# Optimization experiments

Measured on AMD Instinct MI355X. Metric: run time of the kernel, lower is better.

## Reference

```python
import math
import jax, jax.numpy as jnp
import numpy as np

B, H, SQ, SKV, DM = 4, 16, 1024, 1024, 1024
K = 17  # k+1 relative slots
DK = DM // H


def setup_inputs() -> dict:
    key = jax.random.key(0)
    ks = jax.random.split(key, 14)
    n = jax.random.normal
    w_scale = 1.0 / math.sqrt(DM)
    return {
        "query": n(ks[0], (B, SQ, DM), jnp.float32),
        "key": n(ks[1], (B, SKV, DM), jnp.float32),
        "value": n(ks[2], (B, SKV, DM), jnp.float32),
        "pos_enc": n(ks[3], (B, H, K, SKV), jnp.float32),
        "pos_pad": n(ks[4], (B, H, K, SKV), jnp.float32),
        "cross_pos_enc": n(ks[5], (B, H, K, SQ), jnp.float32),
        "cross_pos_pad": n(ks[6], (B, H, K, SQ), jnp.float32),
        "rel_q": n(ks[7], (1, H, 2 * K, DK), jnp.float32) * 0.02,
        "rel_k": n(ks[8], (1, H, 2 * K, DK), jnp.float32) * 0.02,
        "rel_v": n(ks[9], (1, H, 2 * K, DK), jnp.float32) * 0.02,
        "Wq": n(ks[10], (DM, DM), jnp.float32) * w_scale,
        "Wk": n(ks[11], (DM, DM), jnp.float32) * w_scale,
        "Wv": n(ks[12], (DM, DM), jnp.float32) * w_scale,
        "Wo": n(ks[13], (DM, DM), jnp.float32) * w_scale,
    }


def _heads(x, W):
    # nn.Linear(bias=False): y = x @ W.T, then transpose_for_scores -> [B,H,S,DK]
    y = x @ W.T
    b, s, _ = y.shape
    return y.reshape(b, s, H, DK).transpose(0, 2, 1, 3)


def reference(query, key, value, pos_enc, pos_pad, cross_pos_enc, cross_pos_pad,
              rel_q, rel_k, rel_v, Wq, Wk, Wv, Wo):
    q = _heads(query, Wq)   # [B,H,SQ,DK]
    k = _heads(key, Wk)     # [B,H,SKV,DK]
    v = _heads(value, Wv)   # [B,H,SKV,DK]

    # split rel tables: first K rows pair with *_enc, last K rows with *_pad
    rk_e, rk_p = rel_k[0, :, :K], rel_k[0, :, K:]
    rq_e, rq_p = rel_q[0, :, :K], rel_q[0, :, K:]
    rv_e, rv_p = rel_v[0, :, :K], rel_v[0, :, K:]

    # content scores + rel-position bias terms, all [B,H,SQ,SKV]
    scores = jnp.einsum('bhqd,bhsd->bhqs', q, k)
    scores += jnp.einsum('bhqd,hrd,bhrs->bhqs', q, rk_e, pos_enc)
    scores += jnp.einsum('bhqd,hrd,bhrs->bhqs', q, rk_p, pos_pad)
    scores += jnp.einsum('bhsd,hrd,bhrq->bhqs', k, rq_e, cross_pos_enc)
    scores += jnp.einsum('bhsd,hrd,bhrq->bhqs', k, rq_p, cross_pos_pad)

    attn = jax.nn.softmax(scores / math.sqrt(DK), axis=-1)

    out = jnp.einsum('bhqs,bhsd->bhqd', attn, v)
    out += jnp.einsum('bhqs,bhrs,hrd->bhqd', attn, pos_enc, rv_e)
    out += jnp.einsum('bhqs,bhrs,hrd->bhqd', attn, pos_pad, rv_p)

    # finalize_output: merge heads then out_proj
    out = out.transpose(0, 2, 1, 3).reshape(B, SQ, DM)
    return out @ Wo.T
```

## Files before the change

kernel.cpp:

```cpp
#include <hip/hip_runtime.h>
#include <hip/hip_bf16.h>
#include <stdint.h>

typedef float f32x4 __attribute__((ext_vector_type(4)));
typedef __bf16 bf16x8 __attribute__((ext_vector_type(8)));

#define NBH 64
#define SS 1024
#define DAUG 160
#define KAPPA 0.18033688011104293f

static __device__ __forceinline__ unsigned short f2b(float f) {
  union { float f; uint32_t u; } v; v.f = f;
  return (unsigned short)((v.u + 0x7fffu + ((v.u >> 16) & 1u)) >> 16);
}
static __device__ __forceinline__ float b2f(unsigned short s) {
  union { uint32_t u; float f; } v; v.u = ((uint32_t)s) << 16;
  return v.f;
}

static __device__ __forceinline__ void async16(const void* g, void* l) {
  __builtin_amdgcn_global_load_lds(
      (const __attribute__((address_space(1))) uint32_t*)g,
      (__attribute__((address_space(3))) uint32_t*)l, 16, 0, 0);
}

template <int CTRL>
static __device__ __forceinline__ float dppmaxstep(float x) {
  int y = __builtin_amdgcn_update_dpp(__builtin_bit_cast(int, x), __builtin_bit_cast(int, x),
                                      CTRL, 0xF, 0xF, false);
  return fmaxf(x, __builtin_bit_cast(float, y));
}
static __device__ __forceinline__ float rowmax16(float x) {
  x = dppmaxstep<0x128>(x);
  x = dppmaxstep<0x124>(x);
  x = dppmaxstep<0x122>(x);
  x = dppmaxstep<0x121>(x);
  return x;
}

__global__ void convert7(const float* q, const float* k, const float* v,
                         const float* wq, const float* wk, const float* wv, const float* wo,
                         unsigned short* xq, unsigned short* xk, unsigned short* xv,
                         unsigned short* bwq, unsigned short* bwk, unsigned short* bwv,
                         unsigned short* bwo) {
  const float* s; unsigned short* d; int n;
  switch (blockIdx.y) {
    case 0: s = q;  d = xq;  n = 4194304; break;
    case 1: s = k;  d = xk;  n = 4194304; break;
    case 2: s = v;  d = xv;  n = 4194304; break;
    case 3: s = wq; d = bwq; n = 1048576; break;
    case 4: s = wk; d = bwk; n = 1048576; break;
    case 5: s = wv; d = bwv; n = 1048576; break;
    default: s = wo; d = bwo; n = 1048576; break;
  }
  int n4 = n >> 2;
  for (int i = blockIdx.x * blockDim.x + threadIdx.x; i < n4; i += gridDim.x * blockDim.x) {
    float4 f = ((const float4*)s)[i];
    ushort4 o;
    o.x = f2b(f.x); o.y = f2b(f.y); o.z = f2b(f.z); o.w = f2b(f.w);
    ((ushort4*)d)[i] = o;
  }
}

__global__ __launch_bounds__(256) void proj_qkv(
    const unsigned short* __restrict__ Xq, const unsigned short* __restrict__ Xk,
    const unsigned short* __restrict__ Xv, const unsigned short* __restrict__ Wqb,
    const unsigned short* __restrict__ Wkb, const unsigned short* __restrict__ Wvb,
    unsigned short* __restrict__ Qt, unsigned short* __restrict__ Kt,
    unsigned short* __restrict__ Vp) {
  const int z = blockIdx.z;
  const unsigned short* A = (z == 0) ? Xq : (z == 1) ? Xk : Xv;
  const unsigned short* Bw = (z == 0) ? Wqb : (z == 1) ? Wkb : Wvb;
  unsigned short* Dst = (z == 0) ? Qt : (z == 1) ? Kt : Vp;
  const int dstride = (z == 2) ? 64 : DAUG;
  const float sc = (z == 0) ? KAPPA : 1.0f;

  __shared__ unsigned short At[2][128 * 32];
  __shared__ unsigned short Bt[2][128 * 32];

  const int tid = threadIdx.x, wave = tid >> 6, lane = tid & 63;
  const int r15 = lane & 15, g4 = lane >> 4;
  const int i0 = blockIdx.x * 128, j0 = blockIdx.y * 128;
  const int wm = (wave >> 1) * 64, wn = (wave & 1) * 64;

  auto stage = [&](int k0, int buf) {
#pragma unroll
    for (int c = 0; c < 2; ++c) {
      int ch = (wave * 2 + c) * 64 + lane;
      int row = ch >> 2, cg = ch & 3;
      async16(A + (size_t)(i0 + row) * 1024 + k0 + cg * 8, &At[buf][0] + (wave * 2 + c) * 512);
      async16(Bw + (size_t)(j0 + row) * 1024 + k0 + cg * 8, &Bt[buf][0] + (wave * 2 + c) * 512);
    }
  };

  f32x4 acc[4][4];
#pragma unroll
  for (int m = 0; m < 4; ++m)
#pragma unroll
    for (int n = 0; n < 4; ++n) acc[m][n] = (f32x4){0.f, 0.f, 0.f, 0.f};

  stage(0, 0);
  __syncthreads();

  for (int it = 0; it < 32; ++it) {
    const int cur = it & 1, nxt = cur ^ 1;
    if (it < 31) stage((it + 1) * 32, nxt);
    bf16x8 af[4], bf[4];
#pragma unroll
    for (int m = 0; m < 4; ++m)
      af[m] = *(const bf16x8*)(&At[cur][(wm + m * 16 + r15) * 32 + g4 * 8]);
#pragma unroll
    for (int n = 0; n < 4; ++n)
      bf[n] = *(const bf16x8*)(&Bt[cur][(wn + n * 16 + r15) * 32 + g4 * 8]);
    __builtin_amdgcn_s_setprio(1);
#pragma unroll
    for (int m = 0; m < 4; ++m)
#pragma unroll
      for (int n = 0; n < 4; ++n)
        acc[m][n] = __builtin_amdgcn_mfma_f32_16x16x32_bf16(af[m], bf[n], acc[m][n], 0, 0, 0);
    __builtin_amdgcn_s_setprio(0);
    __syncthreads();
  }

#pragma unroll
  for (int m = 0; m < 4; ++m)
#pragma unroll
    for (int n = 0; n < 4; ++n)
#pragma unroll
      for (int r = 0; r < 4; ++r) {
        int i = i0 + wm + m * 16 + g4 * 4 + r;
        int j = j0 + wn + n * 16 + r15;
        int b = i >> 10, s = i & 1023, h = j >> 6, d = j & 63;
        Dst[(((size_t)b * 16 + h) * SS + s) * dstride + d] = f2b(acc[m][n][r] * sc);
      }
}

__global__ __launch_bounds__(256) void gemm_out(const unsigned short* __restrict__ Oh,
                                                const unsigned short* __restrict__ Wob,
                                                float* __restrict__ Out) {
  __shared__ unsigned short At[2][128 * 32];
  __shared__ unsigned short Bt[2][128 * 32];

  const int tid = threadIdx.x, wave = tid >> 6, lane = tid & 63;
  const int r15 = lane & 15, g4 = lane >> 4;
  const int i0 = blockIdx.x * 128, j0 = blockIdx.y * 128;
  const int wm = (wave >> 1) * 64, wn = (wave & 1) * 64;

  auto stage = [&](int k0, int buf) {
#pragma unroll
    for (int c = 0; c < 2; ++c) {
      int ch = (wave * 2 + c) * 64 + lane;
      int row = ch >> 2, cg = ch & 3;
      int i = i0 + row, b = i >> 10, s = i & 1023;
      int kcol = k0 + cg * 8, h = kcol >> 6, dd = kcol & 63;
      async16(Oh + (((size_t)b * 16 + h) * SS + s) * 64 + dd, &At[buf][0] + (wave * 2 + c) * 512);
      async16(Wob + (size_t)(j0 + row) * 1024 + k0 + cg * 8, &Bt[buf][0] + (wave * 2 + c) * 512);
    }
  };

  f32x4 acc[4][4];
#pragma unroll
  for (int m = 0; m < 4; ++m)
#pragma unroll
    for (int n = 0; n < 4; ++n) acc[m][n] = (f32x4){0.f, 0.f, 0.f, 0.f};

  stage(0, 0);
  __syncthreads();

  for (int it = 0; it < 32; ++it) {
    const int cur = it & 1, nxt = cur ^ 1;
    if (it < 31) stage((it + 1) * 32, nxt);
    bf16x8 af[4], bf[4];
#pragma unroll
    for (int m = 0; m < 4; ++m)
      af[m] = *(const bf16x8*)(&At[cur][(wm + m * 16 + r15) * 32 + g4 * 8]);
#pragma unroll
    for (int n = 0; n < 4; ++n)
      bf[n] = *(const bf16x8*)(&Bt[cur][(wn + n * 16 + r15) * 32 + g4 * 8]);
    __builtin_amdgcn_s_setprio(1);
#pragma unroll
    for (int m = 0; m < 4; ++m)
#pragma unroll
      for (int n = 0; n < 4; ++n)
        acc[m][n] = __builtin_amdgcn_mfma_f32_16x16x32_bf16(af[m], bf[n], acc[m][n], 0, 0, 0);
    __builtin_amdgcn_s_setprio(0);
    __syncthreads();
  }

#pragma unroll
  for (int m = 0; m < 4; ++m)
#pragma unroll
    for (int n = 0; n < 4; ++n)
#pragma unroll
      for (int r = 0; r < 4; ++r) {
        int i = i0 + wm + m * 16 + g4 * 4 + r;
        int j = j0 + wn + n * 16 + r15;
        Out[(size_t)i * 1024 + j] = acc[m][n][r];
      }
}

__global__ __launch_bounds__(256) void aug_dots_mfma2(unsigned short* __restrict__ Qt,
                                                      unsigned short* __restrict__ Kt,
                                                      const float* __restrict__ relk,
                                                      const float* __restrict__ relq) {
  const int z = blockIdx.z;
  unsigned short* T = z ? Kt : Qt;
  const float* rel = z ? relq : relk;
  const int cbase = z ? 98 : 64;
  const int bh = blockIdx.y, h = bh & 15, s0 = blockIdx.x * 128;
  const int tid = threadIdx.x, wave = tid >> 6, lane = tid & 63;
  const int r15 = lane & 15, g4 = lane >> 4;

  __shared__ unsigned short RL[48 * 72];
  for (int idx = tid; idx < 48 * 64; idx += 256) {
    int r = idx >> 6, d = idx & 63;
    RL[r * 72 + d] = (r < 34) ? f2b(rel[((size_t)h * 34 + r) * 64 + d]) : (unsigned short)0;
  }
  __syncthreads();

  bf16x8 bfr[3][2];
#pragma unroll
  for (int n = 0; n < 3; ++n)
#pragma unroll
    for (int st = 0; st < 2; ++st)
      bfr[n][st] = *(const bf16x8*)(RL + (n * 16 + r15) * 72 + st * 32 + g4 * 8);

  f32x4 acc[2][3];
#pragma unroll
  for (int m = 0; m < 2; ++m)
#pragma unroll
    for (int n = 0; n < 3; ++n) acc[m][n] = (f32x4){0.f, 0.f, 0.f, 0.f};

#pragma unroll
  for (int m = 0; m < 2; ++m) {
    const unsigned short* Arow = T + ((size_t)bh * SS + s0 + wave * 32 + m * 16 + r15) * DAUG;
    bf16x8 a0 = *(const bf16x8*)(Arow + g4 * 8);
    bf16x8 a1 = *(const bf16x8*)(Arow + 32 + g4 * 8);
#pragma unroll
    for (int n = 0; n < 3; ++n) {
      acc[m][n] = __builtin_amdgcn_mfma_f32_16x16x32_bf16(a0, bfr[n][0], acc[m][n], 0, 0, 0);
      acc[m][n] = __builtin_amdgcn_mfma_f32_16x16x32_bf16(a1, bfr[n][1], acc[m][n], 0, 0, 0);
    }
  }

#pragma unroll
  for (int m = 0; m < 2; ++m)
#pragma unroll
    for (int n = 0; n < 3; ++n) {
      int col = n * 16 + r15;
      if (col < 34) {
#pragma unroll
        for (int r = 0; r < 4; ++r) {
          int row = s0 + wave * 32 + m * 16 + g4 * 4 + r;
          T[((size_t)bh * SS + row) * DAUG + cbase + col] = f2b(acc[m][n][r]);
        }
      }
    }
}

__global__ __launch_bounds__(256) void pos_copy2(unsigned short* __restrict__ Qt,
                                                 unsigned short* __restrict__ Kt,
                                                 const float* __restrict__ cpe,
                                                 const float* __restrict__ cpp,
                                                 const float* __restrict__ pe,
                                                 const float* __restrict__ pp) {
  const int z = blockIdx.z;
  unsigned short* T = z ? Kt : Qt;
  const float* Pe = z ? pe : cpe;
  const float* Pp = z ? pp : cpp;
  const int cbase = z ? 64 : 98;
  const float scale = z ? 1.0f : KAPPA;
  const int bh = blockIdx.y, s0 = blockIdx.x * 64;
  const int tid = threadIdx.x;
  __shared__ float PeL[17][65];
  __shared__ float PpL[17][65];

  for (int idx = tid; idx < 17 * 64; idx += 256) {
    int r = idx >> 6, c = idx & 63;
    PeL[r][c] = Pe[((size_t)bh * 17 + r) * SS + s0 + c];
    PpL[r][c] = Pp[((size_t)bh * 17 + r) * SS + s0 + c];
  }
  __syncthreads();

  for (int idx = tid; idx < 4096; idx += 256) {
    int s = idx >> 6, j = idx & 63;
    if (j < 34) {
      float v = (j < 17) ? PeL[j][s] : PpL[j - 17][s];
      T[((size_t)bh * SS + s0 + s) * DAUG + cbase + j] = f2b(v * scale);
    } else if (j < 62) {
      T[((size_t)bh * SS + s0 + s) * DAUG + 132 + (j - 34)] = 0;
    }
  }
}

__global__ __launch_bounds__(256) void vprime_T(const unsigned short* __restrict__ Vp,
                                                const float* __restrict__ Pe,
                                                const float* __restrict__ Pp,
                                                const float* __restrict__ relv,
                                                unsigned short* __restrict__ VpT) {
  const int bh = blockIdx.y, h = bh & 15, s0 = blockIdx.x * 64;
  const int tid = threadIdx.x;
  __shared__ float PeL[17][65];
  __shared__ float PpL[17][65];
  __shared__ unsigned short VT[64][72];

  for (int idx = tid; idx < 17 * 64; idx += 256) {
    int r = idx >> 6, c = idx & 63;
    PeL[r][c] = Pe[((size_t)bh * 17 + r) * SS + s0 + c];
    PpL[r][c] = Pp[((size_t)bh * 17 + r) * SS + s0 + c];
  }
  __syncthreads();

  const int d = tid & 63, sg = tid >> 6;
  float acc[16];
#pragma unroll
  for (int si = 0; si < 16; ++si) acc[si] = 0.f;
  for (int r = 0; r < 17; ++r) {
    float ve = relv[((size_t)h * 34 + r) * 64 + d];
    float vpv = relv[((size_t)h * 34 + 17 + r) * 64 + d];
#pragma unroll
    for (int si = 0; si < 16; ++si) {
      int s = sg * 16 + si;
      acc[si] += PeL[r][s] * ve + PpL[r][s] * vpv;
    }
  }
#pragma unroll
  for (int si = 0; si < 16; ++si) {
    int s = sg * 16 + si;
    float v = b2f(Vp[((size_t)bh * SS + s0 + s) * 64 + d]) + acc[si];
    VT[d][s] = f2b(v);
  }
  __syncthreads();

  for (int c = tid; c < 512; c += 256) {
    int row = c >> 3, c8 = c & 7;
    uint4 v = *(const uint4*)&VT[row][c8 * 8];
    *(uint4*)(VpT + ((size_t)bh * 80 + row) * 1024 + s0 + c8 * 8) = v;
  }
  if (tid < 128) {
    int row = 64 + (tid >> 3), c8 = tid & 7;
    uint32_t w = (row == 64) ? 0x3F803F80u : 0u;
    uint4 v = {w, w, w, w};
    *(uint4*)(VpT + ((size_t)bh * 80 + row) * 1024 + s0 + c8 * 8) = v;
  }
}

__global__ __launch_bounds__(512, 4) void flash_attn3(
    const unsigned short* __restrict__ Qt, const unsigned short* __restrict__ Kt,
    const unsigned short* __restrict__ VpT, unsigned short* __restrict__ Oh) {
  const int bh = blockIdx.y;
  const int q0 = blockIdx.x * 128;
  const int tid = threadIdx.x, wave = tid >> 6, lane = tid & 63;
  const int r15 = lane & 15, g4 = lane >> 4;

  __shared__ unsigned short Ks[2][64 * 160];
  __shared__ unsigned short Vs[2][80 * 64];
  __shared__ unsigned short Ps[128 * 72];

  const unsigned short* Kbase = Kt + (size_t)bh * SS * DAUG;
  const unsigned short* Vbase = VpT + (size_t)bh * 80 * 1024;

  bf16x8 qf[5];
  {
    const unsigned short* Qg = Qt + ((size_t)bh * SS + q0 + wave * 16 + r15) * DAUG;
#pragma unroll
    for (int kk = 0; kk < 5; ++kk) qf[kk] = *(const bf16x8*)(Qg + kk * 32 + g4 * 8);
  }

  auto stageK = [&](int kv0, int buf) {
    const unsigned short* Kg = Kbase + (size_t)kv0 * DAUG;
#pragma unroll
    for (int j = 0; j < 2; ++j) {
      int ibase = j * 512 + wave * 64;
      int i = ibase + lane;
      int row = i / 20, c = i % 20;
      int cs = (c < 16) ? (c ^ (row & 7)) : (16 + ((c & 3) ^ (row & 3)));
      async16(Kg + (size_t)row * DAUG + cs * 8, &Ks[buf][0] + (size_t)ibase * 8);
    }
    if (wave < 4) {
      int ibase = 1024 + wave * 64;
      int i = ibase + lane;
      int row = i / 20, c = i % 20;
      int cs = (c < 16) ? (c ^ (row & 7)) : (16 + ((c & 3) ^ (row & 3)));
      async16(Kg + (size_t)row * DAUG + cs * 8, &Ks[buf][0] + (size_t)ibase * 8);
    }
  };
  auto stageV = [&](int kv0, int buf) {
    {
      int c = tid;
      int row = c >> 3, c8 = c & 7;
      async16(Vbase + (size_t)row * 1024 + kv0 + ((c8 ^ (row & 7)) << 3),
              &Vs[buf][0] + (size_t)c * 8);
    }
    if (tid < 128) {
      int c = 512 + tid;
      int row = c >> 3, c8 = c & 7;
      async16(Vbase + (size_t)row * 1024 + kv0 + ((c8 ^ (row & 7)) << 3),
              &Vs[buf][0] + (size_t)c * 8);
    }
  };

  stageK(0, 0);
  stageV(0, 0);
  __syncthreads();

  f32x4 accO[5];
#pragma unroll
  for (int df = 0; df < 5; ++df) accO[df] = (f32x4){0.f, 0.f, 0.f, 0.f};
  float run_m[4] = {-INFINITY, -INFINITY, -INFINITY, -INFINITY};

  for (int t = 0; t < 16; ++t) {
    const int cur = t & 1, nxt = cur ^ 1;
    if (t < 15) {
      stageK((t + 1) * 64, nxt);
      stageV((t + 1) * 64, nxt);
    }

    f32x4 s[4];
#pragma unroll
    for (int f = 0; f < 4; ++f) s[f] = (f32x4){0.f, 0.f, 0.f, 0.f};
    __builtin_amdgcn_s_setprio(1);
#pragma unroll
    for (int f = 0; f < 4; ++f) {
      int row = f * 16 + r15;
#pragma unroll
      for (int kk = 0; kk < 5; ++kk) {
        int c = kk * 4 + g4;
        int cs = (c < 16) ? (c ^ (row & 7)) : (16 + ((c & 3) ^ (row & 3)));
        bf16x8 kf = *(const bf16x8*)(&Ks[cur][(size_t)row * DAUG + cs * 8]);
        s[f] = __builtin_amdgcn_mfma_f32_16x16x32_bf16(qf[kk], kf, s[f], 0, 0, 0);
      }
    }
    __builtin_amdgcn_s_setprio(0);

    float mx[4];
#pragma unroll
    for (int r = 0; r < 4; ++r)
      mx[r] = rowmax16(fmaxf(fmaxf(s[0][r], s[1][r]), fmaxf(s[2][r], s[3][r])));

    bool stable = (mx[0] <= run_m[0] + 8.f) && (mx[1] <= run_m[1] + 8.f) &&
                  (mx[2] <= run_m[2] + 8.f) && (mx[3] <= run_m[3] + 8.f);
    if (!__all(stable)) {
#pragma unroll
      for (int r = 0; r < 4; ++r) {
        float mnew = fmaxf(run_m[r], mx[r]);
        float corr = exp2f(run_m[r] - mnew);
        run_m[r] = mnew;
#pragma unroll
        for (int df = 0; df < 5; ++df) accO[df][r] *= corr;
      }
    }
#pragma unroll
    for (int r = 0; r < 4; ++r)
#pragma unroll
      for (int f = 0; f < 4; ++f) s[f][r] = exp2f(s[f][r] - run_m[r]);

#pragma unroll
    for (int f = 0; f < 4; ++f)
#pragma unroll
      for (int r = 0; r < 4; ++r)
        ((__bf16*)Ps)[(wave * 16 + g4 * 4 + r) * 72 + f * 16 + r15] = (__bf16)s[f][r];

    __builtin_amdgcn_s_setprio(1);
#pragma unroll
    for (int ks = 0; ks < 2; ++ks) {
      bf16x8 pa = *(const bf16x8*)(Ps + (wave * 16 + r15) * 72 + ks * 32 + g4 * 8);
#pragma unroll
      for (int df = 0; df < 5; ++df) {
        int row = df * 16 + r15;
        bf16x8 vb = *(const bf16x8*)(&Vs[cur][(size_t)row * 64 + (((ks * 4 + g4) ^ (r15 & 7)) << 3)]);
        accO[df] = __builtin_amdgcn_mfma_f32_16x16x32_bf16(pa, vb, accO[df], 0, 0, 0);
      }
    }
    __builtin_amdgcn_s_setprio(0);

    __syncthreads();
  }

  float rl[4];
#pragma unroll
  for (int r = 0; r < 4; ++r) {
    float l = __shfl(accO[4][r], lane & 48, 64);
    rl[r] = 1.f / l;
  }
#pragma unroll
  for (int df = 0; df < 4; ++df)
#pragma unroll
    for (int r = 0; r < 4; ++r) {
      float o = accO[df][r] * rl[r];
      Oh[((size_t)bh * SS + q0 + wave * 16 + g4 * 4 + r) * 64 + df * 16 + r15] = f2b(o);
    }
}

extern "C" void kernel_launch(void* const* d_in, const int* in_sizes, int n_in,
                              void* d_out, int out_size, void* d_ws, size_t ws_size,
                              hipStream_t stream) {
  const float* query = (const float*)d_in[0];
  const float* key = (const float*)d_in[1];
  const float* value = (const float*)d_in[2];
  const float* pe = (const float*)d_in[3];
  const float* pp = (const float*)d_in[4];
  const float* cpe = (const float*)d_in[5];
  const float* cpp = (const float*)d_in[6];
  const float* relq = (const float*)d_in[7];
  const float* relk = (const float*)d_in[8];
  const float* relv = (const float*)d_in[9];
  const float* Wq = (const float*)d_in[10];
  const float* Wk = (const float*)d_in[11];
  const float* Wv = (const float*)d_in[12];
  const float* Wo = (const float*)d_in[13];
  float* out = (float*)d_out;
  char* ws = (char*)d_ws;

  unsigned short* Xq = (unsigned short*)(ws + 0);
  unsigned short* Xk = (unsigned short*)(ws + 8388608);
  unsigned short* Xv = (unsigned short*)(ws + 16777216);
  unsigned short* Wqb = (unsigned short*)(ws + 25165824);
  unsigned short* Wkb = (unsigned short*)(ws + 27262976);
  unsigned short* Wvb = (unsigned short*)(ws + 29360128);
  unsigned short* Wob = (unsigned short*)(ws + 31457280);
  unsigned short* Qt = (unsigned short*)(ws + 33554432);
  unsigned short* Kt = (unsigned short*)(ws + 54525952);
  unsigned short* Vp = (unsigned short*)(ws + 75497472);
  unsigned short* Oh = (unsigned short*)(ws + 0);
  unsigned short* VpT = (unsigned short*)(ws + 8388608);

  convert7<<<dim3(1024, 7, 1), 256, 0, stream>>>(query, key, value, Wq, Wk, Wv, Wo, Xq, Xk, Xv,
                                                 Wqb, Wkb, Wvb, Wob);
  proj_qkv<<<dim3(32, 8, 3), 256, 0, stream>>>(Xq, Xk, Xv, Wqb, Wkb, Wvb, Qt, Kt, Vp);
  aug_dots_mfma2<<<dim3(8, 64, 2), 256, 0, stream>>>(Qt, Kt, relk, relq);
  pos_copy2<<<dim3(16, 64, 2), 256, 0, stream>>>(Qt, Kt, cpe, cpp, pe, pp);
  vprime_T<<<dim3(16, 64, 1), 256, 0, stream>>>(Vp, pe, pp, relv, VpT);
  flash_attn3<<<dim3(8, 64, 1), 512, 0, stream>>>(Qt, Kt, VpT, Oh);
  gemm_out<<<dim3(32, 8, 1), 256, 0, stream>>>(Oh, Wob, out);
}
```

Measured before the change: 177.1 us.

## Double flash-attention query tile per wave and remap GEMM block order

The flash attention kernel now gives each wave 32 query rows instead of 16. Each K/V tile loaded into shared memory is reused across 256 queries per block, which halves the K/V staging traffic and the number of blocks. The projection and output GEMMs remap the block index so that consecutive blocks are spread across XCDs and tile groups, aiming at better L2 locality. The trade-off is more registers per thread and only 256 attention blocks, which may reduce occupancy and leave compute units underfilled.

Result: slower. 180.7 us (+2.1%).

```diff
diff --git a/kernel.cpp b/kernel.cpp
--- a/kernel.cpp
+++ b/kernel.cpp
@@ -69,7 +69,10 @@
     const unsigned short* __restrict__ Wkb, const unsigned short* __restrict__ Wvb,
     unsigned short* __restrict__ Qt, unsigned short* __restrict__ Kt,
     unsigned short* __restrict__ Vp) {
-  const int z = blockIdx.z;
+  const int n_ = blockIdx.x + 32 * (blockIdx.y + 8 * blockIdx.z);
+  const int o_ = (n_ & 7) * 96 + (n_ >> 3);
+  const int bx = o_ & 31, by = (o_ >> 5) & 7, z = o_ >> 8;
+
   const unsigned short* A = (z == 0) ? Xq : (z == 1) ? Xk : Xv;
   const unsigned short* Bw = (z == 0) ? Wqb : (z == 1) ? Wkb : Wvb;
   unsigned short* Dst = (z == 0) ? Qt : (z == 1) ? Kt : Vp;
@@ -81,7 +84,7 @@
 
   const int tid = threadIdx.x, wave = tid >> 6, lane = tid & 63;
   const int r15 = lane & 15, g4 = lane >> 4;
-  const int i0 = blockIdx.x * 128, j0 = blockIdx.y * 128;
+  const int i0 = bx * 128, j0 = by * 128;
   const int wm = (wave >> 1) * 64, wn = (wave & 1) * 64;
 
   auto stage = [&](int k0, int buf) {
@@ -139,12 +142,16 @@
 __global__ __launch_bounds__(256) void gemm_out(const unsigned short* __restrict__ Oh,
                                                 const unsigned short* __restrict__ Wob,
                                                 float* __restrict__ Out) {
+  const int n_ = blockIdx.x + 32 * blockIdx.y;
+  const int o_ = (n_ & 7) * 32 + (n_ >> 3);
+  const int bx = o_ & 31, by = o_ >> 5;
+
   __shared__ unsigned short At[2][128 * 32];
   __shared__ unsigned short Bt[2][128 * 32];
 
   const int tid = threadIdx.x, wave = tid >> 6, lane = tid & 63;
   const int r15 = lane & 15, g4 = lane >> 4;
-  const int i0 = blockIdx.x * 128, j0 = blockIdx.y * 128;
+  const int i0 = bx * 128, j0 = by * 128;
   const int wm = (wave >> 1) * 64, wn = (wave & 1) * 64;
 
   auto stage = [&](int k0, int buf) {
@@ -346,26 +353,28 @@
   }
 }
 
-__global__ __launch_bounds__(512, 4) void flash_attn3(
+__global__ __launch_bounds__(512) void flash_attn4(
     const unsigned short* __restrict__ Qt, const unsigned short* __restrict__ Kt,
     const unsigned short* __restrict__ VpT, unsigned short* __restrict__ Oh) {
   const int bh = blockIdx.y;
-  const int q0 = blockIdx.x * 128;
+  const int q0 = blockIdx.x * 256;
   const int tid = threadIdx.x, wave = tid >> 6, lane = tid & 63;
   const int r15 = lane & 15, g4 = lane >> 4;
 
   __shared__ unsigned short Ks[2][64 * 160];
   __shared__ unsigned short Vs[2][80 * 64];
-  __shared__ unsigned short Ps[128 * 72];
+  __shared__ unsigned short Ps[256 * 72];
 
   const unsigned short* Kbase = Kt + (size_t)bh * SS * DAUG;
   const unsigned short* Vbase = VpT + (size_t)bh * 80 * 1024;
 
-  bf16x8 qf[5];
-  {
-    const unsigned short* Qg = Qt + ((size_t)bh * SS + q0 + wave * 16 + r15) * DAUG;
-#pragma unroll
-    for (int kk = 0; kk < 5; ++kk) qf[kk] = *(const bf16x8*)(Qg + kk * 32 + g4 * 8);
+  bf16x8 qf[2][5];
+#pragma unroll
+  for (int sub = 0; sub < 2; ++sub) {
+    const unsigned short* Qg =
+        Qt + ((size_t)bh * SS + q0 + wave * 32 + sub * 16 + r15) * DAUG;
+#pragma unroll
+    for (int kk = 0; kk < 5; ++kk) qf[sub][kk] = *(const bf16x8*)(Qg + kk * 32 + g4 * 8);
   }
 
   auto stageK = [&](int kv0, int buf) {
@@ -405,10 +414,13 @@
   stageV(0, 0);
   __syncthreads();
 
-  f32x4 accO[5];
-#pragma unroll
-  for (int df = 0; df < 5; ++df) accO[df] = (f32x4){0.f, 0.f, 0.f, 0.f};
-  float run_m[4] = {-INFINITY, -INFINITY, -INFINITY, -INFINITY};
+  f32x4 accO[2][5];
+#pragma unroll
+  for (int sub = 0; sub < 2; ++sub)
+#pragma unroll
+    for (int df = 0; df < 5; ++df) accO[sub][df] = (f32x4){0.f, 0.f, 0.f, 0.f};
+  float run_m[2][4] = {{-INFINITY, -INFINITY, -INFINITY, -INFINITY},
+                       {-INFINITY, -INFINITY, -INFINITY, -INFINITY}};
 
   for (int t = 0; t < 16; ++t) {
     const int cur = t & 1, nxt = cur ^ 1;
@@ -417,9 +429,11 @@
       stageV((t + 1) * 64, nxt);
     }
 
-    f32x4 s[4];
-#pragma unroll
-    for (int f = 0; f < 4; ++f) s[f] = (f32x4){0.f, 0.f, 0.f, 0.f};
+    f32x4 s[2][4];
+#pragma unroll
+    for (int sub = 0; sub < 2; ++sub)
+#pragma unroll
+      for (int f = 0; f < 4; ++f) s[sub][f] = (f32x4){0.f, 0.f, 0.f, 0.f};
     __builtin_amdgcn_s_setprio(1);
 #pragma unroll
     for (int f = 0; f < 4; ++f) {
@@ -429,48 +443,65 @@
         int c = kk * 4 + g4;
         int cs = (c < 16) ? (c ^ (row & 7)) : (16 + ((c & 3) ^ (row & 3)));
         bf16x8 kf = *(const bf16x8*)(&Ks[cur][(size_t)row * DAUG + cs * 8]);
-        s[f] = __builtin_amdgcn_mfma_f32_16x16x32_bf16(qf[kk], kf, s[f], 0, 0, 0);
+        s[0][f] = __builtin_amdgcn_mfma_f32_16x16x32_bf16(qf[0][kk], kf, s[0][f], 0, 0, 0);
+        s[1][f] = __builtin_amdgcn_mfma_f32_16x16x32_bf16(qf[1][kk], kf, s[1][f], 0, 0, 0);
       }
     }
     __builtin_amdgcn_s_setprio(0);
 
-    float mx[4];
-#pragma unroll
-    for (int r = 0; r < 4; ++r)
-      mx[r] = rowmax16(fmaxf(fmaxf(s[0][r], s[1][r]), fmaxf(s[2][r], s[3][r])));
-
-    bool stable = (mx[0] <= run_m[0] + 8.f) && (mx[1] <= run_m[1] + 8.f) &&
-                  (mx[2] <= run_m[2] + 8.f) && (mx[3] <= run_m[3] + 8.f);
+    float mx[2][4];
+#pragma unroll
+    for (int sub = 0; sub < 2; ++sub)
+#pragma unroll
+      for (int r = 0; r < 4; ++r)
+        mx[sub][r] = rowmax16(
+            fmaxf(fmaxf(s[sub][0][r], s[sub][1][r]), fmaxf(s[sub][2][r], s[sub][3][r])));
+
+    bool stable = true;
+#pragma unroll
+    for (int sub = 0; sub < 2; ++sub)
+#pragma unroll
+      for (int r = 0; r < 4; ++r) stable = stable && (mx[sub][r] <= run_m[sub][r] + 8.f);
     if (!__all(stable)) {
 #pragma unroll
-      for (int r = 0; r < 4; ++r) {
-        float mnew = fmaxf(run_m[r], mx[r]);
-        float corr = exp2f(run_m[r] - mnew);
-        run_m[r] = mnew;
-#pragma unroll
-        for (int df = 0; df < 5; ++df) accO[df][r] *= corr;
-      }
-    }
-#pragma unroll
-    for (int r = 0; r < 4; ++r)
-#pragma unroll
-      for (int f = 0; f < 4; ++f) s[f][r] = exp2f(s[f][r] - run_m[r]);
-
-#pragma unroll
-    for (int f = 0; f < 4; ++f)
+      for (int sub = 0; sub < 2; ++sub)
+#pragma unroll
+        for (int r = 0; r < 4; ++r) {
+          float mnew = fmaxf(run_m[sub][r], mx[sub][r]);
+          float corr = exp2f(run_m[sub][r] - mnew);
+          run_m[sub][r] = mnew;
+#pragma unroll
+          for (int df = 0; df < 5; ++df) accO[sub][df][r] *= corr;
+        }
+    }
+#pragma unroll
+    for (int sub = 0; sub < 2; ++sub)
 #pragma unroll
       for (int r = 0; r < 4; ++r)
-        ((__bf16*)Ps)[(wave * 16 + g4 * 4 + r) * 72 + f * 16 + r15] = (__bf16)s[f][r];
+#pragma unroll
+        for (int f = 0; f < 4; ++f) s[sub][f][r] = exp2f(s[sub][f][r] - run_m[sub][r]);
+
+#pragma unroll
+    for (int sub = 0; sub < 2; ++sub)
+#pragma unroll
+      for (int f = 0; f < 4; ++f)
+#pragma unroll
+        for (int r = 0; r < 4; ++r)
+          ((__bf16*)Ps)[(wave * 32 + sub * 16 + g4 * 4 + r) * 72 + f * 16 + r15] =
+              (__bf16)s[sub][f][r];
 
     __builtin_amdgcn_s_setprio(1);
 #pragma unroll
     for (int ks = 0; ks < 2; ++ks) {
-      bf16x8 pa = *(const bf16x8*)(Ps + (wave * 16 + r15) * 72 + ks * 32 + g4 * 8);
+      bf16x8 pa0 = *(const bf16x8*)(Ps + (wave * 32 + r15) * 72 + ks * 32 + g4 * 8);
+      bf16x8 pa1 = *(const bf16x8*)(Ps + (wave * 32 + 16 + r15) * 72 + ks * 32 + g4 * 8);
 #pragma unroll
       for (int df = 0; df < 5; ++df) {
         int row = df * 16 + r15;
-        bf16x8 vb = *(const bf16x8*)(&Vs[cur][(size_t)row * 64 + (((ks * 4 + g4) ^ (r15 & 7)) << 3)]);
-        accO[df] = __builtin_amdgcn_mfma_f32_16x16x32_bf16(pa, vb, accO[df], 0, 0, 0);
+        bf16x8 vb =
+            *(const bf16x8*)(&Vs[cur][(size_t)row * 64 + (((ks * 4 + g4) ^ (r15 & 7)) << 3)]);
+        accO[0][df] = __builtin_amdgcn_mfma_f32_16x16x32_bf16(pa0, vb, accO[0][df], 0, 0, 0);
+        accO[1][df] = __builtin_amdgcn_mfma_f32_16x16x32_bf16(pa1, vb, accO[1][df], 0, 0, 0);
       }
     }
     __builtin_amdgcn_s_setprio(0);
@@ -478,19 +509,23 @@
     __syncthreads();
   }
 
-  float rl[4];
-#pragma unroll
-  for (int r = 0; r < 4; ++r) {
-    float l = __shfl(accO[4][r], lane & 48, 64);
-    rl[r] = 1.f / l;
-  }
-#pragma unroll
-  for (int df = 0; df < 4; ++df)
+#pragma unroll
+  for (int sub = 0; sub < 2; ++sub) {
+    float rl[4];
 #pragma unroll
     for (int r = 0; r < 4; ++r) {
-      float o = accO[df][r] * rl[r];
-      Oh[((size_t)bh * SS + q0 + wave * 16 + g4 * 4 + r) * 64 + df * 16 + r15] = f2b(o);
-    }
+      float l = __shfl(accO[sub][4][r], lane & 48, 64);
+      rl[r] = 1.f / l;
+    }
+#pragma unroll
+    for (int df = 0; df < 4; ++df)
+#pragma unroll
+      for (int r = 0; r < 4; ++r) {
+        float o = accO[sub][df][r] * rl[r];
+        Oh[((size_t)bh * SS + q0 + wave * 32 + sub * 16 + g4 * 4 + r) * 64 + df * 16 + r15] =
+            f2b(o);
+      }
+  }
 }
 
 extern "C" void kernel_launch(void* const* d_in, const int* in_sizes, int n_in,
@@ -532,6 +567,6 @@
   aug_dots_mfma2<<<dim3(8, 64, 2), 256, 0, stream>>>(Qt, Kt, relk, relq);
   pos_copy2<<<dim3(16, 64, 2), 256, 0, stream>>>(Qt, Kt, cpe, cpp, pe, pp);
   vprime_T<<<dim3(16, 64, 1), 256, 0, stream>>>(Vp, pe, pp, relv, VpT);
-  flash_attn3<<<dim3(8, 64, 1), 512, 0, stream>>>(Qt, Kt, VpT, Oh);
+  flash_attn4<<<dim3(4, 64, 1), 512, 0, stream>>>(Qt, Kt, VpT, Oh);
   gemm_out<<<dim3(32, 8, 1), 256, 0, stream>>>(Oh, Wob, out);
 }
```

## Fuse relative-position dot products into QKV projection and merge pos/vprime kernels

Applied to the files above, without the earlier changes.

The q·rel_k and k·rel_q dot products are now computed in the projection GEMM epilogue. Each tile is staged in swizzled shared memory and multiplied by the rel tables with MFMA, which removes a separate kernel that re-read Q and K from global memory. The pos_copy and vprime_T kernels are merged into one launch that shares the loaded pos tiles. Block indices in both GEMMs are remapped, likely for better L2 locality. This cuts launches and global traffic at the cost of more shared memory and a longer epilogue in the projection kernel.

Measured after the change: 173.0 us. 2.3% less time.

```diff
diff --git a/kernel.cpp b/kernel.cpp
--- a/kernel.cpp
+++ b/kernel.cpp
@@ -68,29 +68,47 @@
     const unsigned short* __restrict__ Xv, const unsigned short* __restrict__ Wqb,
     const unsigned short* __restrict__ Wkb, const unsigned short* __restrict__ Wvb,
     unsigned short* __restrict__ Qt, unsigned short* __restrict__ Kt,
-    unsigned short* __restrict__ Vp) {
-  const int z = blockIdx.z;
+    unsigned short* __restrict__ Vp, const float* __restrict__ relk,
+    const float* __restrict__ relq) {
+  const int n_ = blockIdx.x + 32 * (blockIdx.y + 8 * blockIdx.z);
+  const int o_ = (n_ & 7) * 96 + (n_ >> 3);
+  const int bx = o_ & 31, by = (o_ >> 5) & 7, z = o_ >> 8;
+
   const unsigned short* A = (z == 0) ? Xq : (z == 1) ? Xk : Xv;
   const unsigned short* Bw = (z == 0) ? Wqb : (z == 1) ? Wkb : Wvb;
   unsigned short* Dst = (z == 0) ? Qt : (z == 1) ? Kt : Vp;
   const int dstride = (z == 2) ? 64 : DAUG;
   const float sc = (z == 0) ? KAPPA : 1.0f;
 
-  __shared__ unsigned short At[2][128 * 32];
-  __shared__ unsigned short Bt[2][128 * 32];
+  __shared__ unsigned short SMEM[23296];
+  unsigned short* AtB = SMEM;
+  unsigned short* BtB = SMEM + 8192;
+  unsigned short* RelL = SMEM + 16384;
+  unsigned short* Ys = SMEM;
 
   const int tid = threadIdx.x, wave = tid >> 6, lane = tid & 63;
   const int r15 = lane & 15, g4 = lane >> 4;
-  const int i0 = blockIdx.x * 128, j0 = blockIdx.y * 128;
+  const int i0 = bx * 128, j0 = by * 128;
   const int wm = (wave >> 1) * 64, wn = (wave & 1) * 64;
+
+  if (z < 2) {
+    const float* rel = (z == 0) ? relk : relq;
+    const int h0 = by * 2;
+    for (int idx = tid; idx < 2 * 48 * 64; idx += 256) {
+      int hh = idx / (48 * 64), rem = idx % (48 * 64);
+      int r = rem >> 6, d = rem & 63;
+      float v = (r < 34) ? rel[(((size_t)(h0 + hh)) * 34 + r) * 64 + d] : 0.f;
+      RelL[(hh * 48 + r) * 72 + d] = f2b(v);
+    }
+  }
 
   auto stage = [&](int k0, int buf) {
 #pragma unroll
     for (int c = 0; c < 2; ++c) {
       int ch = (wave * 2 + c) * 64 + lane;
       int row = ch >> 2, cg = ch & 3;
-      async16(A + (size_t)(i0 + row) * 1024 + k0 + cg * 8, &At[buf][0] + (wave * 2 + c) * 512);
-      async16(Bw + (size_t)(j0 + row) * 1024 + k0 + cg * 8, &Bt[buf][0] + (wave * 2 + c) * 512);
+      async16(A + (size_t)(i0 + row) * 1024 + k0 + cg * 8, AtB + buf * 4096 + (wave * 2 + c) * 512);
+      async16(Bw + (size_t)(j0 + row) * 1024 + k0 + cg * 8, BtB + buf * 4096 + (wave * 2 + c) * 512);
     }
   };
 
@@ -109,10 +127,10 @@
     bf16x8 af[4], bf[4];
 #pragma unroll
     for (int m = 0; m < 4; ++m)
-      af[m] = *(const bf16x8*)(&At[cur][(wm + m * 16 + r15) * 32 + g4 * 8]);
+      af[m] = *(const bf16x8*)(AtB + cur * 4096 + (wm + m * 16 + r15) * 32 + g4 * 8);
 #pragma unroll
     for (int n = 0; n < 4; ++n)
-      bf[n] = *(const bf16x8*)(&Bt[cur][(wn + n * 16 + r15) * 32 + g4 * 8]);
+      bf[n] = *(const bf16x8*)(BtB + cur * 4096 + (wn + n * 16 + r15) * 32 + g4 * 8);
     __builtin_amdgcn_s_setprio(1);
 #pragma unroll
     for (int m = 0; m < 4; ++m)
@@ -129,22 +147,82 @@
     for (int n = 0; n < 4; ++n)
 #pragma unroll
       for (int r = 0; r < 4; ++r) {
-        int i = i0 + wm + m * 16 + g4 * 4 + r;
-        int j = j0 + wn + n * 16 + r15;
+        int lrow = wm + m * 16 + g4 * 4 + r;
+        int lcol = wn + n * 16 + r15;
+        int i = i0 + lrow, j = j0 + lcol;
+        float y = acc[m][n][r] * sc;
         int b = i >> 10, s = i & 1023, h = j >> 6, d = j & 63;
-        Dst[(((size_t)b * 16 + h) * SS + s) * dstride + d] = f2b(acc[m][n][r] * sc);
-      }
+        Dst[(((size_t)b * 16 + h) * SS + s) * dstride + d] = f2b(y);
+        if (z < 2) {
+          int c8 = (lcol >> 3) ^ (lrow & 7);
+          Ys[lrow * 128 + c8 * 8 + (lcol & 7)] = f2b(y);
+        }
+      }
+
+  if (z < 2) {
+    const int cbase = (z == 0) ? 64 : 98;
+    __syncthreads();
+#pragma unroll
+    for (int hh = 0; hh < 2; ++hh) {
+      bf16x8 bfr[3][2];
+#pragma unroll
+      for (int n = 0; n < 3; ++n)
+#pragma unroll
+        for (int st = 0; st < 2; ++st)
+          bfr[n][st] = *(const bf16x8*)(RelL + (hh * 48 + n * 16 + r15) * 72 + st * 32 + g4 * 8);
+
+      f32x4 a2[2][3];
+#pragma unroll
+      for (int m2 = 0; m2 < 2; ++m2)
+#pragma unroll
+        for (int n = 0; n < 3; ++n) a2[m2][n] = (f32x4){0.f, 0.f, 0.f, 0.f};
+
+#pragma unroll
+      for (int m2 = 0; m2 < 2; ++m2) {
+        int lrow = wave * 32 + m2 * 16 + r15;
+        int c8a = (hh * 8 + 0 * 4 + g4) ^ (lrow & 7);
+        int c8b = (hh * 8 + 1 * 4 + g4) ^ (lrow & 7);
+        bf16x8 a0 = *(const bf16x8*)(Ys + lrow * 128 + c8a * 8);
+        bf16x8 a1 = *(const bf16x8*)(Ys + lrow * 128 + c8b * 8);
+#pragma unroll
+        for (int n = 0; n < 3; ++n) {
+          a2[m2][n] = __builtin_amdgcn_mfma_f32_16x16x32_bf16(a0, bfr[n][0], a2[m2][n], 0, 0, 0);
+          a2[m2][n] = __builtin_amdgcn_mfma_f32_16x16x32_bf16(a1, bfr[n][1], a2[m2][n], 0, 0, 0);
+        }
+      }
+
+      const int h = by * 2 + hh;
+#pragma unroll
+      for (int m2 = 0; m2 < 2; ++m2)
+#pragma unroll
+        for (int n = 0; n < 3; ++n) {
+          int col = n * 16 + r15;
+          if (col < 34) {
+#pragma unroll
+            for (int rr = 0; rr < 4; ++rr) {
+              int i = i0 + wave * 32 + m2 * 16 + g4 * 4 + rr;
+              int b = i >> 10, s = i & 1023;
+              Dst[(((size_t)b * 16 + h) * SS + s) * DAUG + cbase + col] = f2b(a2[m2][n][rr]);
+            }
+          }
+        }
+    }
+  }
 }
 
 __global__ __launch_bounds__(256) void gemm_out(const unsigned short* __restrict__ Oh,
                                                 const unsigned short* __restrict__ Wob,
                                                 float* __restrict__ Out) {
+  const int n_ = blockIdx.x + 32 * blockIdx.y;
+  const int o_ = (n_ & 7) * 32 + (n_ >> 3);
+  const int bx = o_ & 31, by = o_ >> 5;
+
   __shared__ unsigned short At[2][128 * 32];
   __shared__ unsigned short Bt[2][128 * 32];
 
   const int tid = threadIdx.x, wave = tid >> 6, lane = tid & 63;
   const int r15 = lane & 15, g4 = lane >> 4;
-  const int i0 = blockIdx.x * 128, j0 = blockIdx.y * 128;
+  const int i0 = bx * 128, j0 = by * 128;
   const int wm = (wave >> 1) * 64, wn = (wave & 1) * 64;
 
   auto stage = [&](int k0, int buf) {
@@ -200,81 +278,26 @@
       }
 }
 
-__global__ __launch_bounds__(256) void aug_dots_mfma2(unsigned short* __restrict__ Qt,
-                                                      unsigned short* __restrict__ Kt,
-                                                      const float* __restrict__ relk,
-                                                      const float* __restrict__ relq) {
-  const int z = blockIdx.z;
-  unsigned short* T = z ? Kt : Qt;
-  const float* rel = z ? relq : relk;
-  const int cbase = z ? 98 : 64;
-  const int bh = blockIdx.y, h = bh & 15, s0 = blockIdx.x * 128;
-  const int tid = threadIdx.x, wave = tid >> 6, lane = tid & 63;
-  const int r15 = lane & 15, g4 = lane >> 4;
-
-  __shared__ unsigned short RL[48 * 72];
-  for (int idx = tid; idx < 48 * 64; idx += 256) {
-    int r = idx >> 6, d = idx & 63;
-    RL[r * 72 + d] = (r < 34) ? f2b(rel[((size_t)h * 34 + r) * 64 + d]) : (unsigned short)0;
-  }
-  __syncthreads();
-
-  bf16x8 bfr[3][2];
-#pragma unroll
-  for (int n = 0; n < 3; ++n)
-#pragma unroll
-    for (int st = 0; st < 2; ++st)
-      bfr[n][st] = *(const bf16x8*)(RL + (n * 16 + r15) * 72 + st * 32 + g4 * 8);
-
-  f32x4 acc[2][3];
-#pragma unroll
-  for (int m = 0; m < 2; ++m)
-#pragma unroll
-    for (int n = 0; n < 3; ++n) acc[m][n] = (f32x4){0.f, 0.f, 0.f, 0.f};
-
-#pragma unroll
-  for (int m = 0; m < 2; ++m) {
-    const unsigned short* Arow = T + ((size_t)bh * SS + s0 + wave * 32 + m * 16 + r15) * DAUG;
-    bf16x8 a0 = *(const bf16x8*)(Arow + g4 * 8);
-    bf16x8 a1 = *(const bf16x8*)(Arow + 32 + g4 * 8);
-#pragma unroll
-    for (int n = 0; n < 3; ++n) {
-      acc[m][n] = __builtin_amdgcn_mfma_f32_16x16x32_bf16(a0, bfr[n][0], acc[m][n], 0, 0, 0);
-      acc[m][n] = __builtin_amdgcn_mfma_f32_16x16x32_bf16(a1, bfr[n][1], acc[m][n], 0, 0, 0);
-    }
-  }
-
-#pragma unroll
-  for (int m = 0; m < 2; ++m)
-#pragma unroll
-    for (int n = 0; n < 3; ++n) {
-      int col = n * 16 + r15;
-      if (col < 34) {
-#pragma unroll
-        for (int r = 0; r < 4; ++r) {
-          int row = s0 + wave * 32 + m * 16 + g4 * 4 + r;
-          T[((size_t)bh * SS + row) * DAUG + cbase + col] = f2b(acc[m][n][r]);
-        }
-      }
-    }
-}
-
-__global__ __launch_bounds__(256) void pos_copy2(unsigned short* __restrict__ Qt,
-                                                 unsigned short* __restrict__ Kt,
-                                                 const float* __restrict__ cpe,
-                                                 const float* __restrict__ cpp,
-                                                 const float* __restrict__ pe,
-                                                 const float* __restrict__ pp) {
+__global__ __launch_bounds__(256) void pos_vp(unsigned short* __restrict__ Qt,
+                                              unsigned short* __restrict__ Kt,
+                                              const float* __restrict__ cpe,
+                                              const float* __restrict__ cpp,
+                                              const float* __restrict__ pe,
+                                              const float* __restrict__ pp,
+                                              const unsigned short* __restrict__ Vp,
+                                              const float* __restrict__ relv,
+                                              unsigned short* __restrict__ VpT) {
   const int z = blockIdx.z;
   unsigned short* T = z ? Kt : Qt;
   const float* Pe = z ? pe : cpe;
   const float* Pp = z ? pp : cpp;
   const int cbase = z ? 64 : 98;
   const float scale = z ? 1.0f : KAPPA;
-  const int bh = blockIdx.y, s0 = blockIdx.x * 64;
+  const int bh = blockIdx.y, h = bh & 15, s0 = blockIdx.x * 64;
   const int tid = threadIdx.x;
   __shared__ float PeL[17][65];
   __shared__ float PpL[17][65];
+  __shared__ unsigned short VT[64][72];
 
   for (int idx = tid; idx < 17 * 64; idx += 256) {
     int r = idx >> 6, c = idx & 63;
@@ -292,57 +315,40 @@
       T[((size_t)bh * SS + s0 + s) * DAUG + 132 + (j - 34)] = 0;
     }
   }
-}
-
-__global__ __launch_bounds__(256) void vprime_T(const unsigned short* __restrict__ Vp,
-                                                const float* __restrict__ Pe,
-                                                const float* __restrict__ Pp,
-                                                const float* __restrict__ relv,
-                                                unsigned short* __restrict__ VpT) {
-  const int bh = blockIdx.y, h = bh & 15, s0 = blockIdx.x * 64;
-  const int tid = threadIdx.x;
-  __shared__ float PeL[17][65];
-  __shared__ float PpL[17][65];
-  __shared__ unsigned short VT[64][72];
-
-  for (int idx = tid; idx < 17 * 64; idx += 256) {
-    int r = idx >> 6, c = idx & 63;
-    PeL[r][c] = Pe[((size_t)bh * 17 + r) * SS + s0 + c];
-    PpL[r][c] = Pp[((size_t)bh * 17 + r) * SS + s0 + c];
-  }
-  __syncthreads();
-
-  const int d = tid & 63, sg = tid >> 6;
-  float acc[16];
-#pragma unroll
-  for (int si = 0; si < 16; ++si) acc[si] = 0.f;
-  for (int r = 0; r < 17; ++r) {
-    float ve = relv[((size_t)h * 34 + r) * 64 + d];
-    float vpv = relv[((size_t)h * 34 + 17 + r) * 64 + d];
+
+  if (z == 1) {
+    const int d = tid & 63, sg = tid >> 6;
+    float acc[16];
+#pragma unroll
+    for (int si = 0; si < 16; ++si) acc[si] = 0.f;
+    for (int r = 0; r < 17; ++r) {
+      float ve = relv[((size_t)h * 34 + r) * 64 + d];
+      float vpv = relv[((size_t)h * 34 + 17 + r) * 64 + d];
+#pragma unroll
+      for (int si = 0; si < 16; ++si) {
+        int s = sg * 16 + si;
+        acc[si] += PeL[r][s] * ve + PpL[r][s] * vpv;
+      }
+    }
 #pragma unroll
     for (int si = 0; si < 16; ++si) {
       int s = sg * 16 + si;
-      acc[si] += PeL[r][s] * ve + PpL[r][s] * vpv;
-    }
-  }
-#pragma unroll
-  for (int si = 0; si < 16; ++si) {
-    int s = sg * 16 + si;
-    float v = b2f(Vp[((size_t)bh * SS + s0 + s) * 64 + d]) + acc[si];
-    VT[d][s] = f2b(v);
-  }
-  __syncthreads();
-
-  for (int c = tid; c < 512; c += 256) {
-    int row = c >> 3, c8 = c & 7;
-    uint4 v = *(const uint4*)&VT[row][c8 * 8];
-    *(uint4*)(VpT + ((size_t)bh * 80 + row) * 1024 + s0 + c8 * 8) = v;
-  }
-  if (tid < 128) {
-    int row = 64 + (tid >> 3), c8 = tid & 7;
-    uint32_t w = (row == 64) ? 0x3F803F80u : 0u;
-    uint4 v = {w, w, w, w};
-    *(uint4*)(VpT + ((size_t)bh * 80 + row) * 1024 + s0 + c8 * 8) = v;
+      float v = b2f(Vp[((size_t)bh * SS + s0 + s) * 64 + d]) + acc[si];
+      VT[d][s] = f2b(v);
+    }
+    __syncthreads();
+
+    for (int c = tid; c < 512; c += 256) {
+      int row = c >> 3, c8 = c & 7;
+      uint4 v = *(const uint4*)&VT[row][c8 * 8];
+      *(uint4*)(VpT + ((size_t)bh * 80 + row) * 1024 + s0 + c8 * 8) = v;
+    }
+    if (tid < 128) {
+      int row = 64 + (tid >> 3), c8 = tid & 7;
+      uint32_t w = (row == 64) ? 0x3F803F80u : 0u;
+      uint4 v = {w, w, w, w};
+      *(uint4*)(VpT + ((size_t)bh * 80 + row) * 1024 + s0 + c8 * 8) = v;
+    }
   }
 }
 
@@ -528,10 +534,8 @@
 
   convert7<<<dim3(1024, 7, 1), 256, 0, stream>>>(query, key, value, Wq, Wk, Wv, Wo, Xq, Xk, Xv,
                                                  Wqb, Wkb, Wvb, Wob);
-  proj_qkv<<<dim3(32, 8, 3), 256, 0, stream>>>(Xq, Xk, Xv, Wqb, Wkb, Wvb, Qt, Kt, Vp);
-  aug_dots_mfma2<<<dim3(8, 64, 2), 256, 0, stream>>>(Qt, Kt, relk, relq);
-  pos_copy2<<<dim3(16, 64, 2), 256, 0, stream>>>(Qt, Kt, cpe, cpp, pe, pp);
-  vprime_T<<<dim3(16, 64, 1), 256, 0, stream>>>(Vp, pe, pp, relv, VpT);
+  proj_qkv<<<dim3(32, 8, 3), 256, 0, stream>>>(Xq, Xk, Xv, Wqb, Wkb, Wvb, Qt, Kt, Vp, relk, relq);
+  pos_vp<<<dim3(16, 64, 2), 256, 0, stream>>>(Qt, Kt, cpe, cpp, pe, pp, Vp, relv, VpT);
   flash_attn3<<<dim3(8, 64, 1), 512, 0, stream>>>(Qt, Kt, VpT, Oh);
   gemm_out<<<dim3(32, 8, 1), 256, 0, stream>>>(Oh, Wob, out);
 }
```
